# Optimization experiments

Hardware: AMD Instinct MI355X
Metric: run time of the kernel (lower is better)

Reference implementation:

```python
import jax, jax.numpy as jnp
import numpy as np

MAX_PATCHES = 1024  # init kwarg max_patches


def _patch_lengths_static(seq_len: int, max_patches: int) -> np.ndarray:
    """Exact trace-time emulation of the original sequential fill loop.

    Replicates call(): fill patches 0..max_patches-2 with avg_patch_size while
    remaining > avg, break-and-set if remaining <= avg, then the final
    'if remaining > 0' writes the leftover into the last slot (including the
    original's behavior where a break leaves 'remaining' unchanged and it is
    ALSO written to the last slot). Lengths depend only on seq_len (static),
    so they are identical for every batch row.
    """
    avg = max(seq_len // max_patches, 1)
    lengths = np.zeros(max_patches, dtype=np.int32)
    remaining = seq_len
    for p in range(max_patches - 1):
        if remaining <= avg:
            lengths[p] = remaining
            break
        lengths[p] = avg
        remaining -= avg
    if remaining > 0:
        lengths[max_patches - 1] = remaining
    return lengths


def setup_inputs() -> dict:
    key = jax.random.key(0)
    entropy = jax.random.normal(key, (16, 1048576), dtype=jnp.float32)
    return {"entropy": entropy}


def reference(entropy):
    B, S = entropy.shape
    lengths = jnp.asarray(_patch_lengths_static(S, MAX_PATCHES))  # (P,) int32
    patch_lengths = jnp.broadcast_to(lengths[None, :], (B, MAX_PATCHES))  # (B, P)

    # compute_patch_ids, vectorized: patch id of position `pos` is the number
    # of patch-end boundaries <= pos, i.e. right-searchsorted into the cumsum.
    cum = jnp.cumsum(patch_lengths, axis=1)  # (B, P) exclusive-end boundaries
    # max_seq_len = max(sum(lengths)) == S by construction of the fill loop.
    pos = jnp.arange(S, dtype=jnp.int32)  # (S,)
    patch_ids = jax.vmap(lambda c: jnp.searchsorted(c, pos, side="right"))(cum)
    patch_ids = patch_ids.astype(jnp.int32)  # (B, S)

    return patch_lengths, patch_ids
```

## Files before the change

kernel.cpp:

```cpp
#include <hip/hip_runtime.h>


__global__ __launch_bounds__(256) void DynamicPatcher_62448824484363_kernel(
    int* __restrict__ out,
    int BP,
    int total,
    int S,
    int P,
    int avg,
    int nf,
    int breakRem,
    int lastVal)
{
    int t = blockIdx.x * 256 + threadIdx.x;
    int i = t * 4;
    if (i >= total) return;

    int4 v;
    if (i < BP) {
        int p0 = i % P;
        #define LVAL(p) ((p) < nf ? avg : ((p) == P - 1 ? lastVal : ((p) == nf ? breakRem : 0)))
        v.x = LVAL(p0);
        v.y = LVAL(p0 + 1);
        v.z = LVAL(p0 + 2);
        v.w = LVAL(p0 + 3);
        #undef LVAL
    } else {
        int e = i - BP;
        int pos0 = e % S;
        int q = pos0 / avg;
        int r = pos0 - q * avg;
        int a2 = avg + avg;
        int a3 = a2 + avg;
        v.x = min(q, nf);
        v.y = min(q + (r + 1 >= avg) + (r + 1 >= a2) + (r + 1 >= a3), nf);
        v.z = min(q + (r + 2 >= avg) + (r + 2 >= a2) + (r + 2 >= a3), nf);
        v.w = min(q + (r + 3 >= avg) + (r + 3 >= a2) + (r + 3 >= a3), nf);
    }
    *reinterpret_cast<int4*>(out + i) = v;
}

extern "C" void kernel_launch(void* const* d_in, const int* in_sizes, int n_in,
                              void* d_out, int out_size, void* d_ws, size_t ws_size,
                              hipStream_t stream) {
    (void)d_in; (void)n_in; (void)d_ws; (void)ws_size;

    const int P = 1024;
    long long BS = (long long)in_sizes[0];
    long long BPll = (long long)out_size - BS;
    long long B = BPll / P;
    long long S = BS / B;

    long long avgll = S / P;
    if (avgll < 1) avgll = 1;
    int avg = (int)avgll;

    long long nfll = 0;
    if (S > avg) {
        nfll = (S - avg - 1) / avg + 1;
        if (nfll > P - 1) nfll = P - 1;
    }
    int nf = (int)nfll;

    int breakRem = (int)(S - nfll * avg);
    int lastVal;
    if (nf < P - 1) {
        lastVal = breakRem;
    } else {
        long long rf = S - (long long)(P - 1) * avg;
        lastVal = rf > 0 ? (int)rf : 0;
    }

    int total = out_size;
    int threads = total / 4;
    int blocks = (threads + 255) / 256;

    DynamicPatcher_62448824484363_kernel<<<blocks, 256, 0, stream>>>(
        (int*)d_out, (int)BPll, total, (int)S, P, avg, nf, breakRem, lastVal);
}
```

Measured before the change: 102.5 us.

## Use 2D row grid, shift-based patch ids, and 4 stores per thread

The flat 1D grid becomes a 2D grid with one row per batch entry, plus one extra block per row that writes the patch lengths. This removes the per-element modulo by S and the branch between the two output regions. When avg is a power of two, a template specialisation computes patch ids with a shift instead of an integer divide. Each thread now writes four int4 vectors, which cuts the block count. The kernel is store-bandwidth bound (about 64 MB written), so the gains from cheaper arithmetic may be small.

```diff
diff --git a/kernel.cpp b/kernel.cpp
--- a/kernel.cpp
+++ b/kernel.cpp
@@ -1,43 +1,56 @@
 #include <hip/hip_runtime.h>
 
 
+template <bool POW2>
 __global__ __launch_bounds__(256) void DynamicPatcher_62448824484363_kernel(
     int* __restrict__ out,
-    int BP,
-    int total,
-    int S,
-    int P,
-    int avg,
-    int nf,
-    int breakRem,
-    int lastVal)
+    int B, int S, int P,
+    int avg, int sh,
+    int nf, int breakRem, int lastVal,
+    int blocksPerRow)
 {
-    int t = blockIdx.x * 256 + threadIdx.x;
-    int i = t * 4;
-    if (i >= total) return;
+    const int row = blockIdx.y;
 
-    int4 v;
-    if (i < BP) {
-        int p0 = i % P;
-        #define LVAL(p) ((p) < nf ? avg : ((p) == P - 1 ? lastVal : ((p) == nf ? breakRem : 0)))
-        v.x = LVAL(p0);
-        v.y = LVAL(p0 + 1);
-        v.z = LVAL(p0 + 2);
-        v.w = LVAL(p0 + 3);
-        #undef LVAL
-    } else {
-        int e = i - BP;
-        int pos0 = e % S;
-        int q = pos0 / avg;
-        int r = pos0 - q * avg;
-        int a2 = avg + avg;
-        int a3 = a2 + avg;
-        v.x = min(q, nf);
-        v.y = min(q + (r + 1 >= avg) + (r + 1 >= a2) + (r + 1 >= a3), nf);
-        v.z = min(q + (r + 2 >= avg) + (r + 2 >= a2) + (r + 2 >= a3), nf);
-        v.w = min(q + (r + 3 >= avg) + (r + 3 >= a2) + (r + 3 >= a3), nf);
+    if ((int)blockIdx.x == blocksPerRow) {
+        int* lrow = out + (size_t)row * P;
+        for (int i = threadIdx.x * 4; i < P; i += 256 * 4) {
+            int4 v;
+            #define LVAL(p) ((p) < nf ? avg : ((p) == P - 1 ? lastVal : ((p) == nf ? breakRem : 0)))
+            v.x = LVAL(i);
+            v.y = LVAL(i + 1);
+            v.z = LVAL(i + 2);
+            v.w = LVAL(i + 3);
+            #undef LVAL
+            *reinterpret_cast<int4*>(lrow + i) = v;
+        }
+        return;
     }
-    *reinterpret_cast<int4*>(out + i) = v;
+
+    int* irow = out + (size_t)B * P + (size_t)row * S;
+    const int base = blockIdx.x * 4096 + threadIdx.x * 4;
+
+    #pragma unroll
+    for (int u = 0; u < 4; ++u) {
+        int pos = base + u * 1024;
+        if (pos >= S) break;
+        int4 v;
+        if (POW2) {
+            v.x = min(pos >> sh, nf);
+            v.y = min((pos + 1) >> sh, nf);
+            v.z = min((pos + 2) >> sh, nf);
+            v.w = min((pos + 3) >> sh, nf);
+        } else {
+            int q = pos / avg;
+            int r = pos - q * avg;
+            int a2 = avg + avg;
+            int a3 = a2 + avg;
+            v.x = min(q, nf);
+            v.y = min(q + (r + 1 >= avg) + (r + 1 >= a2) + (r + 1 >= a3), nf);
+            v.z = min(q + (r + 2 >= avg) + (r + 2 >= a2) + (r + 2 >= a3), nf);
+            v.w = min(q + (r + 3 >= avg) + (r + 3 >= a2) + (r + 3 >= a3), nf);
+        }
+        *reinterpret_cast<int4*>(irow + pos) = v;
+    }
 }
 
 extern "C" void kernel_launch(void* const* d_in, const int* in_sizes, int n_in,
@@ -48,16 +61,16 @@
     const int P = 1024;
     long long BS = (long long)in_sizes[0];
     long long BPll = (long long)out_size - BS;
-    long long B = BPll / P;
-    long long S = BS / B;
+    int B = (int)(BPll / P);
+    int S = (int)(BS / B);
 
-    long long avgll = S / P;
+    long long avgll = (long long)S / P;
     if (avgll < 1) avgll = 1;
     int avg = (int)avgll;
 
     long long nfll = 0;
     if (S > avg) {
-        nfll = (S - avg - 1) / avg + 1;
+        nfll = ((long long)S - avg - 1) / avg + 1;
         if (nfll > P - 1) nfll = P - 1;
     }
     int nf = (int)nfll;
@@ -67,14 +80,22 @@
     if (nf < P - 1) {
         lastVal = breakRem;
     } else {
-        long long rf = S - (long long)(P - 1) * avg;
+        long long rf = (long long)S - (long long)(P - 1) * avg;
         lastVal = rf > 0 ? (int)rf : 0;
     }
 
-    int total = out_size;
-    int threads = total / 4;
-    int blocks = (threads + 255) / 256;
+    int blocksPerRow = (S + 4095) / 4096;
+    dim3 grid(blocksPerRow + 1, B);
 
-    DynamicPatcher_62448824484363_kernel<<<blocks, 256, 0, stream>>>(
-        (int*)d_out, (int)BPll, total, (int)S, P, avg, nf, breakRem, lastVal);
+    bool pow2 = (avg & (avg - 1)) == 0;
+    int sh = 0;
+    if (pow2) { int a = avg; while (a > 1) { a >>= 1; ++sh; } }
+
+    if (pow2) {
+        DynamicPatcher_62448824484363_kernel<true><<<grid, 256, 0, stream>>>(
+            (int*)d_out, B, S, P, avg, sh, nf, breakRem, lastVal, blocksPerRow);
+    } else {
+        DynamicPatcher_62448824484363_kernel<false><<<grid, 256, 0, stream>>>(
+            (int*)d_out, B, S, P, avg, sh, nf, breakRem, lastVal, blocksPerRow);
+    }
 }
```

Result: no change. 101.5 us (-1.0%).
